# Kernel optimization log

Hardware: AMD Instinct MI355X
Metric: run time of the kernel (lower is better)

## Reference

```python
import jax, jax.numpy as jnp
import numpy as np

N = 50000
E = 800000
IN_CH = 128
OUT_CH = 32
HEADS = 2
NEG_SLOPE = 0.2


def setup_inputs() -> dict:
    key = jax.random.key(0)
    k_x, k_ei, k_w, k_as, k_ad, k_b = jax.random.split(key, 6)
    x = jax.random.normal(k_x, (N, IN_CH), dtype=jnp.float32)
    edge_index = jax.random.randint(k_ei, (2, E), 0, N, dtype=jnp.int64)
    # Glorot-style init scale for linear weight and attention vectors
    w_scale = 1.0 / np.sqrt(IN_CH)
    W = jax.random.normal(k_w, (IN_CH, HEADS * OUT_CH), dtype=jnp.float32) * w_scale
    a_scale = 1.0 / np.sqrt(OUT_CH)
    a_src = jax.random.normal(k_as, (HEADS, OUT_CH), dtype=jnp.float32) * a_scale
    a_dst = jax.random.normal(k_ad, (HEADS, OUT_CH), dtype=jnp.float32) * a_scale
    bias = jnp.zeros((HEADS * OUT_CH,), dtype=jnp.float32)
    return {"x": x, "edge_index": edge_index, "W": W, "a_src": a_src,
            "a_dst": a_dst, "bias": bias}


def reference(x, edge_index, W, a_src, a_dst, bias):
    n = x.shape[0]
    # add self-loops (add_self_loops=True); static shape E+N
    loops = jnp.tile(jnp.arange(n, dtype=edge_index.dtype), (2, 1))
    ei = jnp.concatenate([edge_index, loops], axis=1)
    src, dst = ei[0], ei[1]

    # linear projection -> per-head features [N, H, C]
    h = (x @ W).reshape(n, HEADS, OUT_CH)

    # per-node attention logits [N, H]
    alpha_s = jnp.sum(h * a_src[None], axis=-1)
    alpha_d = jnp.sum(h * a_dst[None], axis=-1)

    # per-edge score, LeakyReLU, segment softmax over edges grouped by dst
    e = jax.nn.leaky_relu(alpha_s[src] + alpha_d[dst], NEG_SLOPE)  # [E', H]
    e_max = jax.ops.segment_max(e, dst, num_segments=n)           # [N, H]
    e_exp = jnp.exp(e - e_max[dst])
    denom = jax.ops.segment_sum(e_exp, dst, num_segments=n)       # [N, H]
    alpha = e_exp / (denom[dst] + 1e-16)                          # [E', H]

    # scatter-add weighted messages [N, H, C]
    out = jax.ops.segment_sum(alpha[:, :, None] * h[src], dst, num_segments=n)
    # concat heads + bias (concat=True)
    return out.reshape(n, HEADS * OUT_CH) + bias
```

## Files before the change

kernel.cpp:

```cpp
#include <hip/hip_runtime.h>
#include <hip/hip_bf16.h>
#include <hip/hip_fp16.h>
#include <math.h>

#define IN_CH   128
#define OUT_CH  32
#define HEADS   2
#define HC      (HEADS * OUT_CH)
#define NEG_SLOPE 0.2f

#define NODE_TILE 64
#define LDS_STRIDE 136

#define BIN_CAP 64

typedef _Float16 h2_t __attribute__((ext_vector_type(2)));
union V16 { int4 v; h2_t h[4]; };

__device__ __forceinline__ float fdot2(h2_t a, h2_t b, float c) {
#if __has_builtin(__builtin_amdgcn_fdot2)
    return __builtin_amdgcn_fdot2(a, b, c, false);
#else
    return c + (float)a.x * (float)b.x + (float)a.y * (float)b.y;
#endif
}

__global__ __launch_bounds__(256) void gemm_hist_kernel(
    const float* __restrict__ x, const float* __restrict__ W,
    const float* __restrict__ a_src, const float* __restrict__ a_dst,
    __half* __restrict__ h, float* __restrict__ alpha_s, float* __restrict__ alpha_d,
    const int* __restrict__ dst, int* __restrict__ deg, int* __restrict__ rank,
    int n_nodes, int n_edges, int n_total, int gemm_blocks)
{
    const int tid = threadIdx.x;

    if (blockIdx.x >= gemm_blocks) {
        int e = (blockIdx.x - gemm_blocks) * blockDim.x + tid;
        if (e < n_total) {
            int d = (e < n_edges) ? dst[e] : (e - n_edges);
            rank[e] = atomicAdd(&deg[d], 1);
        }
        return;
    }

    __shared__ _Float16 Wt[HC * IN_CH];
    __shared__ _Float16 Xs[NODE_TILE * LDS_STRIDE];

    const int node0 = blockIdx.x * NODE_TILE;

    const float4* W4 = (const float4*)W;
    #pragma unroll
    for (int i = 0; i < 8; ++i) {
        int idx4 = tid + i * 256;
        int k  = idx4 >> 4;
        int c4 = idx4 & 15;
        float4 v = W4[idx4];
        int chunk = k >> 3, klo = k & 7;
        _Float16 vals[4] = {(_Float16)v.x, (_Float16)v.y, (_Float16)v.z, (_Float16)v.w};
        #pragma unroll
        for (int r = 0; r < 4; ++r) {
            int col = c4 * 4 + r;
            int gc  = (col >> 3) & 7;
            Wt[col * IN_CH + ((chunk ^ gc) << 3) + klo] = vals[r];
        }
    }

    const float4* X4 = (const float4*)x;
    #pragma unroll
    for (int i = 0; i < 8; ++i) {
        int idx4 = tid + i * 256;
        int r = idx4 >> 5, c4 = idx4 & 31;
        int node = node0 + r;
        float4 v = make_float4(0.f, 0.f, 0.f, 0.f);
        if (node < n_nodes) v = X4[(size_t)node * (IN_CH / 4) + c4];
        _Float16 hv[4] = {(_Float16)v.x, (_Float16)v.y, (_Float16)v.z, (_Float16)v.w};
        *(int2*)&Xs[r * LDS_STRIDE + c4 * 4] = *(int2*)hv;
    }
    __syncthreads();

    const int n    = tid >> 3;
    const int g    = tid & 7;
    const int col0 = g * 8;
    const int head = col0 >> 5;
    const int c0   = col0 & 31;

    float accA[8] = {0,0,0,0,0,0,0,0};
    float accB[8] = {0,0,0,0,0,0,0,0};
    const _Float16* xa = &Xs[n * LDS_STRIDE];
    const _Float16* xb = &Xs[(n + 32) * LDS_STRIDE];

    for (int k0 = 0; k0 < IN_CH; k0 += 8) {
        V16 va, vb;
        va.v = *(const int4*)&xa[k0];
        vb.v = *(const int4*)&xb[k0];
        const _Float16* wbase = &Wt[col0 * IN_CH + ((((k0 >> 3) ^ g)) << 3)];
        #pragma unroll
        for (int j = 0; j < 8; ++j) {
            V16 w;
            w.v = *(const int4*)&wbase[j * IN_CH];
            float a = accA[j], b = accB[j];
            a = fdot2(w.h[0], va.h[0], a); b = fdot2(w.h[0], vb.h[0], b);
            a = fdot2(w.h[1], va.h[1], a); b = fdot2(w.h[1], vb.h[1], b);
            a = fdot2(w.h[2], va.h[2], a); b = fdot2(w.h[2], vb.h[2], b);
            a = fdot2(w.h[3], va.h[3], a); b = fdot2(w.h[3], vb.h[3], b);
            accA[j] = a; accB[j] = b;
        }
    }

    float asr[8], adr[8];
    #pragma unroll
    for (int j = 0; j < 8; ++j) {
        asr[j] = a_src[head * OUT_CH + c0 + j];
        adr[j] = a_dst[head * OUT_CH + c0 + j];
    }

    #pragma unroll
    for (int half = 0; half < 2; ++half) {
        const float* acc = half ? accB : accA;
        const int node = node0 + n + half * 32;
        if (node < n_nodes) {
            unsigned u[8];
            #pragma unroll
            for (int j = 0; j < 8; ++j) u[j] = __half_as_ushort(__float2half_rn(acc[j]));
            int4 v = make_int4((int)(u[0] | (u[1] << 16)), (int)(u[2] | (u[3] << 16)),
                               (int)(u[4] | (u[5] << 16)), (int)(u[6] | (u[7] << 16)));
            *(int4*)&h[(size_t)node * HC + col0] = v;
        }
        float ps = 0.f, pd = 0.f;
        #pragma unroll
        for (int j = 0; j < 8; ++j) { ps += acc[j] * asr[j]; pd += acc[j] * adr[j]; }
        ps += __shfl_xor(ps, 1); ps += __shfl_xor(ps, 2);
        pd += __shfl_xor(pd, 1); pd += __shfl_xor(pd, 2);
        if ((g & 3) == 0 && node < n_nodes) {
            alpha_s[node * HEADS + head] = ps;
            alpha_d[node * HEADS + head] = pd;
        }
    }
}

__global__ void fill_kernel(const int* __restrict__ src, const int* __restrict__ dst,
                            const int* __restrict__ rank,
                            int* __restrict__ bins4, int n_edges, int n_total)
{
    int e = blockIdx.x * blockDim.x + threadIdx.x;
    if (e >= n_total) return;
    int s, d;
    if (e < n_edges) { s = src[e]; d = dst[e]; }
    else             { s = d = e - n_edges; }
    int rk = rank[e];
    if (rk < BIN_CAP) bins4[(size_t)d * BIN_CAP + rk] = s;
}

__global__ __launch_bounds__(256) void node_gather_kernel(
    const int* __restrict__ bins4, const int* __restrict__ deg,
    const float* __restrict__ alpha_s, const float* __restrict__ alpha_d,
    const __half* __restrict__ h, const float* __restrict__ bias,
    float* __restrict__ out, int n_nodes)
{
    __shared__ int2 stage[4][BIN_CAP];
    const int w = threadIdx.x >> 6;
    int node = blockIdx.x * 4 + w;
    if (node >= n_nodes) return;
    const int lane = threadIdx.x & 63;
    int cnt = deg[node];
    if (cnt > BIN_CAP) cnt = BIN_CAP;

    float2 adn = ((const float2*)alpha_d)[node];

    int sreg = 0;
    float p0 = 0.f, p1 = 0.f;
    if (lane < cnt) {
        sreg = bins4[(size_t)node * BIN_CAP + lane];
        float2 a2 = ((const float2*)alpha_s)[sreg];
        float v0 = a2.x + adn.x;
        float v1 = a2.y + adn.y;
        v0 = (v0 > 0.f) ? v0 : NEG_SLOPE * v0;
        v1 = (v1 > 0.f) ? v1 : NEG_SLOPE * v1;
        p0 = __expf(v0);
        p1 = __expf(v1);
    }

    unsigned u0 = __half_as_ushort(__float2half_rn(p0));
    unsigned u1 = __half_as_ushort(__float2half_rn(p1));
    float q0 = __half2float(__ushort_as_half((unsigned short)u0));
    float q1 = __half2float(__ushort_as_half((unsigned short)u1));

    #pragma unroll
    for (int off = 1; off < 64; off <<= 1) {
        q0 += __shfl_xor(q0, off);
        q1 += __shfl_xor(q1, off);
    }

    stage[w][lane] = make_int2(sreg, (int)((u1 << 16) | u0));

    const int eh = lane >> 5;
    const int c2 = lane & 31;
    const unsigned hshift = (unsigned)(c2 >> 4) << 4;
    const unsigned laneofs = (unsigned)c2 << 2;
    const char* hb = (const char*)h;

    float accx = 0.f, accy = 0.f;
    for (int i = 0; i < cnt; i += 8) {
        #pragma unroll
        for (int j = 0; j < 4; ++j) {
            int2 rec = stage[w][i + 2 * j + eh];
            unsigned ofs = ((unsigned)rec.x << 7) + laneofs;
            __half2 hv = *(const __half2*)(hb + ofs);
            float2 hf = __half22float2(hv);
            float pj = __half2float(__ushort_as_half(
                           (unsigned short)(((unsigned)rec.y) >> hshift)));
            accx += pj * hf.x;
            accy += pj * hf.y;
        }
    }
    accx += __shfl_xor(accx, 32);
    accy += __shfl_xor(accy, 32);

    if (lane < 32) {
        const float lsum = (c2 >> 4) ? q1 : q0;
        const float inv = 1.f / (lsum + 1e-16f);
        float2 b2 = ((const float2*)bias)[c2];
        float2 o;
        o.x = accx * inv + b2.x;
        o.y = accy * inv + b2.y;
        ((float2*)out)[(size_t)node * (HC / 2) + c2] = o;
    }
}

extern "C" void kernel_launch(void* const* d_in, const int* in_sizes, int n_in,
                              void* d_out, int out_size, void* d_ws, size_t ws_size,
                              hipStream_t stream)
{
    const float* x      = (const float*)d_in[0];
    const int*   ei     = (const int*)d_in[1];
    const float* W      = (const float*)d_in[2];
    const float* a_src  = (const float*)d_in[3];
    const float* a_dst  = (const float*)d_in[4];
    const float* bias   = (const float*)d_in[5];
    float* out = (float*)d_out;

    const int n_nodes = in_sizes[0] / IN_CH;
    const int n_edges = in_sizes[1] / 2;
    const int n_total = n_edges + n_nodes;

    const int* src = ei;
    const int* dst = ei + n_edges;

    __half* h      = (__half*)d_ws;
    float* alpha_s = (float*)(h + (size_t)n_nodes * HC);
    float* alpha_d = alpha_s + (size_t)n_nodes * HEADS;
    int* deg       = (int*)(alpha_d + (size_t)n_nodes * HEADS);
    int* rank      = deg + n_nodes;
    int* bins4     = rank + n_total;

    const int edge_blocks = (n_total + 255) / 256;
    const int gemm_blocks = (n_nodes + NODE_TILE - 1) / NODE_TILE;

    hipMemsetAsync(deg, 0, (size_t)n_nodes * sizeof(int), stream);

    gemm_hist_kernel<<<gemm_blocks + edge_blocks, 256, 0, stream>>>(
        x, W, a_src, a_dst, h, alpha_s, alpha_d,
        dst, deg, rank, n_nodes, n_edges, n_total, gemm_blocks);

    fill_kernel<<<edge_blocks, 256, 0, stream>>>(
        src, dst, rank, bins4, n_edges, n_total);

    int ng_blocks = (n_nodes + 3) / 4;
    node_gather_kernel<<<ng_blocks, 256, 0, stream>>>(
        bins4, deg, alpha_s, alpha_d, h, bias, out, n_nodes);
}
```

Measured before the change: 152.2 us.

## Swizzle X tile in LDS and widen aggregation gathers to 16-byte loads

The GEMM stage drops the padded LDS stride for the X tile and uses an XOR swizzle on the 16-byte chunk index, matching the existing W layout, to avoid bank conflicts without padding. The aggregation stage changes the lane mapping so each lane loads 8 fp16 features (int4) for one of 8 edges per iteration instead of a half2 per lane, cutting the number of gather instructions. In exchange, the aggregation now needs a three-step cross-lane reduction of 8 accumulators and writes output with only 8 lanes active.

```diff
diff --git a/kernel.cpp b/kernel.cpp
--- a/kernel.cpp
+++ b/kernel.cpp
@@ -10,9 +10,9 @@
 #define NEG_SLOPE 0.2f
 
 #define NODE_TILE 64
-#define LDS_STRIDE 136
 
 #define BIN_CAP 64
+
 
 typedef _Float16 h2_t __attribute__((ext_vector_type(2)));
 union V16 { int4 v; h2_t h[4]; };
@@ -44,7 +44,7 @@
     }
 
     __shared__ _Float16 Wt[HC * IN_CH];
-    __shared__ _Float16 Xs[NODE_TILE * LDS_STRIDE];
+    __shared__ _Float16 Xs[NODE_TILE * IN_CH];
 
     const int node0 = blockIdx.x * NODE_TILE;
 
@@ -74,7 +74,8 @@
         float4 v = make_float4(0.f, 0.f, 0.f, 0.f);
         if (node < n_nodes) v = X4[(size_t)node * (IN_CH / 4) + c4];
         _Float16 hv[4] = {(_Float16)v.x, (_Float16)v.y, (_Float16)v.z, (_Float16)v.w};
-        *(int2*)&Xs[r * LDS_STRIDE + c4 * 4] = *(int2*)hv;
+        int ofs = r * IN_CH + (((c4 >> 1) ^ (r & 7)) << 3) + (c4 & 1) * 4;
+        *(int2*)&Xs[ofs] = *(int2*)hv;
     }
     __syncthreads();
 
@@ -86,14 +87,17 @@
 
     float accA[8] = {0,0,0,0,0,0,0,0};
     float accB[8] = {0,0,0,0,0,0,0,0};
-    const _Float16* xa = &Xs[n * LDS_STRIDE];
-    const _Float16* xb = &Xs[(n + 32) * LDS_STRIDE];
+    const _Float16* xa = &Xs[n * IN_CH];
+    const _Float16* xb = &Xs[(n + 32) * IN_CH];
+    const int xkey = n & 7;
 
     for (int k0 = 0; k0 < IN_CH; k0 += 8) {
+        const int chunk = k0 >> 3;
+        const int xofs  = ((chunk ^ xkey) << 3);
         V16 va, vb;
-        va.v = *(const int4*)&xa[k0];
-        vb.v = *(const int4*)&xb[k0];
-        const _Float16* wbase = &Wt[col0 * IN_CH + ((((k0 >> 3) ^ g)) << 3)];
+        va.v = *(const int4*)&xa[xofs];
+        vb.v = *(const int4*)&xb[xofs];
+        const _Float16* wbase = &Wt[col0 * IN_CH + ((chunk ^ g) << 3)];
         #pragma unroll
         for (int j = 0; j < 8; ++j) {
             V16 w;
@@ -193,37 +197,48 @@
 
     stage[w][lane] = make_int2(sreg, (int)((u1 << 16) | u0));
 
-    const int eh = lane >> 5;
-    const int c2 = lane & 31;
-    const unsigned hshift = (unsigned)(c2 >> 4) << 4;
-    const unsigned laneofs = (unsigned)c2 << 2;
+    const int q = lane >> 3;
+    const int c = lane & 7;
+    const unsigned hshift = (unsigned)(c >> 2) << 4;
+    const unsigned laneofs = (unsigned)c << 4;
     const char* hb = (const char*)h;
 
-    float accx = 0.f, accy = 0.f;
+    float acc[8] = {0,0,0,0,0,0,0,0};
     for (int i = 0; i < cnt; i += 8) {
-        #pragma unroll
-        for (int j = 0; j < 4; ++j) {
-            int2 rec = stage[w][i + 2 * j + eh];
-            unsigned ofs = ((unsigned)rec.x << 7) + laneofs;
-            __half2 hv = *(const __half2*)(hb + ofs);
-            float2 hf = __half22float2(hv);
-            float pj = __half2float(__ushort_as_half(
-                           (unsigned short)(((unsigned)rec.y) >> hshift)));
-            accx += pj * hf.x;
-            accy += pj * hf.y;
-        }
-    }
-    accx += __shfl_xor(accx, 32);
-    accy += __shfl_xor(accy, 32);
-
-    if (lane < 32) {
-        const float lsum = (c2 >> 4) ? q1 : q0;
+        int2 rec = stage[w][i + q];
+        unsigned ofs = ((unsigned)rec.x << 7) + laneofs;
+        int4 hv = *(const int4*)(hb + ofs);
+        float pj = __half2float(__ushort_as_half(
+                       (unsigned short)(((unsigned)rec.y) >> hshift)));
+        const int* hp = &hv.x;
+        #pragma unroll
+        for (int k = 0; k < 4; ++k) {
+            __half2 h2 = *(__half2*)&hp[k];
+            float2 f2 = __half22float2(h2);
+            acc[2*k]   += pj * f2.x;
+            acc[2*k+1] += pj * f2.y;
+        }
+    }
+    #pragma unroll
+    for (int k = 0; k < 8; ++k) {
+        acc[k] += __shfl_xor(acc[k], 8);
+        acc[k] += __shfl_xor(acc[k], 16);
+        acc[k] += __shfl_xor(acc[k], 32);
+    }
+
+    if (lane < 8) {
+        const float lsum = (c >> 2) ? q1 : q0;
         const float inv = 1.f / (lsum + 1e-16f);
-        float2 b2 = ((const float2*)bias)[c2];
-        float2 o;
-        o.x = accx * inv + b2.x;
-        o.y = accy * inv + b2.y;
-        ((float2*)out)[(size_t)node * (HC / 2) + c2] = o;
+        float4 b0 = ((const float4*)bias)[2 * c];
+        float4 b1 = ((const float4*)bias)[2 * c + 1];
+        float4 o0, o1;
+        o0.x = acc[0] * inv + b0.x;  o0.y = acc[1] * inv + b0.y;
+        o0.z = acc[2] * inv + b0.z;  o0.w = acc[3] * inv + b0.w;
+        o1.x = acc[4] * inv + b1.x;  o1.y = acc[5] * inv + b1.y;
+        o1.z = acc[6] * inv + b1.z;  o1.w = acc[7] * inv + b1.w;
+        float4* orow = (float4*)out + (size_t)node * (HC / 4);
+        orow[2 * c]     = o0;
+        orow[2 * c + 1] = o1;
     }
 }
 
```

New measurement: 155.5 us. 2.2% more time.
